# Performance work log

Measured on AMD Instinct MI355X. Metric: run time of the kernel, lower is better.

## Reference

```python
import jax, jax.numpy as jnp
import numpy as np

B, N, J, P = 64, 2048, 32, 64   # instances, ops per instance, jobs, ops per job (N = J*P)
D, H = 128, 128                 # out_size_ope, hidden_size_ope
NEG_SLOPE = 0.2


def _kaiming(key, fan_in, fan_out):
    return jax.random.normal(key, (fan_in, fan_out), jnp.float32) * np.sqrt(2.0 / fan_in)


def _mlp(x, W1, b1, W2, b2):
    # nn.Sequential(Linear, ELU, Linear)
    return jax.nn.elu(x @ W1 + b1) @ W2 + b2


def setup_inputs() -> dict:
    key = jax.random.key(0)
    ks = jax.random.split(key, 4)
    features = jax.random.normal(ks[0], (B, N, D), jnp.float32)
    job_starts = jnp.arange(J, dtype=jnp.int32) * P                      # first op of each job block
    offsets = jax.random.randint(ks[1], (B, J), 0, P)                    # current position within block
    ope_step_batch = job_starts[None, :] + offsets                       # [B, J], step_j in [start_j, end_j]
    end_ope_biases_batch = jnp.broadcast_to(job_starts + (P - 1), (B, J))
    opes_appertain_batch = jnp.broadcast_to(jnp.repeat(jnp.arange(J, dtype=jnp.int32), P)[None, :], (B, N))
    batch_idxes = jnp.arange(B, dtype=jnp.int32)
    inp = {
        'features': features,
        'discount_r': jnp.float32(0.9),
        'ope_step_batch': ope_step_batch,
        'end_ope_biases_batch': end_ope_biases_batch,
        'opes_appertain_batch': opes_appertain_batch,
        'batch_idxes': batch_idxes,
    }
    for i, nm in enumerate(['fw', 'zj', 'pr']):
        k1, k2 = jax.random.split(jax.random.fold_in(ks[2], i))
        inp[nm + '_W1'] = _kaiming(k1, D, H)
        inp[nm + '_b1'] = jnp.zeros((H,), jnp.float32)
        inp[nm + '_W2'] = _kaiming(k2, H, D)
        inp[nm + '_b2'] = jnp.zeros((D,), jnp.float32)
    return inp


def reference(features, discount_r,
              fw_W1, fw_b1, fw_W2, fw_b2,
              zj_W1, zj_b1, zj_W2, zj_b2,
              pr_W1, pr_b1, pr_W2, pr_b2,
              ope_step_batch, end_ope_biases_batch, opes_appertain_batch, batch_idxes):
    # opes_appertain_batch is accepted but unused, exactly like the torch forward.
    f32 = features.dtype
    steps = ope_step_batch[batch_idxes]        # [B, J]
    ends = end_ope_biases_batch[batch_idxes]   # [B, J]
    i = jnp.arange(N)

    # --- per-job descending update loop, vectorized ---
    # op i is updated iff step_j < i <= end_j for its job j; descending order in the
    # original means feat[i-1] is still the ORIGINAL value, so updates are independent.
    memb = (i[None, None, :] > steps[:, :, None]) & (i[None, None, :] <= ends[:, :, None])  # [B,J,N]
    updated = jnp.any(memb, axis=1)                                                         # [B,N]
    step_of = jnp.sum(jnp.where(memb, steps[:, :, None], 0), axis=1)                        # [B,N]
    rpow = discount_r ** (i[None, :] - step_of).astype(f32)                                 # r^(i - step)
    feat_prev = jnp.concatenate([jnp.zeros_like(features[:, :1]), features[:, :-1]], axis=1)
    # aggregate(MEAN): agg_f_w(feat_pre) + agg_f_w(feat_sub * r)
    cand = _mlp(features, fw_W1, fw_b1, fw_W2, fw_b2) + \
           _mlp(feat_prev * rpow[..., None], fw_W1, fw_b1, fw_W2, fw_b2)
    feat1 = jnp.where(updated[..., None], cand, features)

    # --- collect feat at each valid job's current step (step positions are never updated) ---
    collected = jax.vmap(lambda f, s: f[s])(features, steps)   # [B, J, D]
    valid = steps <= ends                                      # [B, J]
    n = jnp.sum(valid, axis=1).astype(f32)                     # [B]
    S = jnp.sum(jnp.where(valid[..., None], collected, 0.0), axis=1)  # [B, D]
    # aggregate_dif: new[j] = agg_z_j((old[j] + r * sum_{k!=j} old[k]) / n)
    mixed = (collected + discount_r * (S[:, None, :] - collected)) / n[:, None, None]
    z = _mlp(mixed, zj_W1, zj_b1, zj_W2, zj_b2)                # [B, J, D]

    # faithful replication of feat_opt[b][save_index[k]] = features_all[k]
    # (writes at op positions equal to JOB indices 0..J-1, for valid jobs)
    head = jnp.where(valid[..., None], z, feat1[:, :J, :])
    feat2 = feat1.at[:, :J, :].set(head)

    out = jax.nn.leaky_relu(_mlp(feat2, pr_W1, pr_b1, pr_W2, pr_b2), NEG_SLOPE)
    return out
```

## Files before the change

### kernel.cpp

```cpp
#include <hip/hip_runtime.h>

#define B_ 64
#define N_ 2048
#define J_ 32
#define D_ 128
#define NEG_SLOPE_ 0.2f

typedef __attribute__((ext_vector_type(4))) float f32x4;
typedef __attribute__((ext_vector_type(8))) __bf16 bf16x8;
typedef __attribute__((ext_vector_type(4))) __bf16 bf16x4;

#define ACT_NONE 0
#define ACT_ELU 1
#define ACT_LEAKY 2

template<int ACT>
__device__ __forceinline__ float apply_act(float v) {
    if constexpr (ACT == ACT_ELU)        return v > 0.f ? v : __expf(v) - 1.f;
    else if constexpr (ACT == ACT_LEAKY) return v >= 0.f ? v : NEG_SLOPE_ * v;
    else return v;
}

__device__ __forceinline__ bf16x8 frag_ld(const __bf16* src, int row, int kc) {
    return *(const bf16x8*)&src[row * D_ + ((kc ^ (row & 7)) << 3)];
}

__device__ __forceinline__ void load_wregs2(const __bf16* __restrict__ wmat,
                                            int wst, int ln, int lq, bf16x8 wr_[4][2]) {
#pragma unroll
    for (int ks = 0; ks < 4; ++ks)
#pragma unroll
        for (int mt = 0; mt < 2; ++mt)
            wr_[ks][mt] = frag_ld(wmat, wst * 32 + mt * 16 + ln, ks * 4 + lq);
}

__device__ __forceinline__ void gemmS(const __bf16* xb, const bf16x8 wr_[4][2],
                                      int ln, int lq, f32x4 acc[2][4]) {
    const f32x4 z = {0.f, 0.f, 0.f, 0.f};
#pragma unroll
    for (int mt = 0; mt < 2; ++mt)
#pragma unroll
        for (int nt = 0; nt < 4; ++nt) acc[mt][nt] = z;
#pragma unroll
    for (int ks = 0; ks < 4; ++ks) {
        const int kc = ks * 4 + lq;
        bf16x8 b[4];
#pragma unroll
        for (int nt = 0; nt < 4; ++nt) b[nt] = frag_ld(xb, nt * 16 + ln, kc);
#pragma unroll
        for (int mt = 0; mt < 2; ++mt)
#pragma unroll
            for (int nt = 0; nt < 4; ++nt)
                acc[mt][nt] = __builtin_amdgcn_mfma_f32_16x16x32_bf16(wr_[ks][mt], b[nt], acc[mt][nt], 0, 0, 0);
    }
}

__device__ __forceinline__ void gemmS32(const __bf16* xb, const bf16x8 wr_[4][2],
                                        int ln, int lq, f32x4 acc[2][2]) {
    const f32x4 z = {0.f, 0.f, 0.f, 0.f};
#pragma unroll
    for (int mt = 0; mt < 2; ++mt) { acc[mt][0] = z; acc[mt][1] = z; }
#pragma unroll
    for (int ks = 0; ks < 4; ++ks) {
        const int kc = ks * 4 + lq;
        const bf16x8 b0 = frag_ld(xb, ln, kc);
        const bf16x8 b1 = frag_ld(xb, 16 + ln, kc);
#pragma unroll
        for (int mt = 0; mt < 2; ++mt) {
            acc[mt][0] = __builtin_amdgcn_mfma_f32_16x16x32_bf16(wr_[ks][mt], b0, acc[mt][0], 0, 0, 0);
            acc[mt][1] = __builtin_amdgcn_mfma_f32_16x16x32_bf16(wr_[ks][mt], b1, acc[mt][1], 0, 0, 0);
        }
    }
}

template<int ACT>
__device__ __forceinline__ void epiS_lds(const f32x4 acc[2][4], __bf16* dst,
                                         const float* __restrict__ bias,
                                         int wst, int ln, int lq) {
#pragma unroll
    for (int mt = 0; mt < 2; ++mt) {
        const int cb = wst * 32 + mt * 16 + lq * 4;
        const f32x4 bv = *(const f32x4*)&bias[cb];
#pragma unroll
        for (int nt = 0; nt < 4; ++nt) {
            const int jr = nt * 16 + ln;
            bf16x4 o;
#pragma unroll
            for (int r = 0; r < 4; ++r)
                o[r] = (__bf16)apply_act<ACT>(acc[mt][nt][r] + bv[r]);
            *(bf16x4*)&dst[jr * D_ + (((cb >> 3) ^ (jr & 7)) << 3) + (cb & 7)] = o;
        }
    }
}

template<int ACT>
__device__ __forceinline__ void epiS32_lds(const f32x4 acc[2][2], __bf16* dst, int rowoff,
                                           const float* __restrict__ bias,
                                           int wst, int ln, int lq) {
#pragma unroll
    for (int mt = 0; mt < 2; ++mt) {
        const int cb = wst * 32 + mt * 16 + lq * 4;
        const f32x4 bv = *(const f32x4*)&bias[cb];
#pragma unroll
        for (int nt = 0; nt < 2; ++nt) {
            const int jr = rowoff + nt * 16 + ln;
            bf16x4 o;
#pragma unroll
            for (int r = 0; r < 4; ++r)
                o[r] = (__bf16)apply_act<ACT>(acc[mt][nt][r] + bv[r]);
            *(bf16x4*)&dst[jr * D_ + (((cb >> 3) ^ (jr & 7)) << 3) + (cb & 7)] = o;
        }
    }
}

__global__ __launch_bounds__(256) void k_prep(
    const float* __restrict__ w0, const float* __restrict__ w1,
    const float* __restrict__ w2, const float* __restrict__ w3,
    const float* __restrict__ w4, const float* __restrict__ w5,
    __bf16* __restrict__ wdst,
    const float* __restrict__ F, const int* __restrict__ STEP,
    const int* __restrict__ ENDB, const int* __restrict__ BIDX,
    float* __restrict__ Sbuf, int* __restrict__ nvalid) {
    const int t = threadIdx.x;
    if (blockIdx.x < 6) {
        const float* src;
        switch (blockIdx.x) {
            case 0: src = w0; break; case 1: src = w1; break; case 2: src = w2; break;
            case 3: src = w3; break; case 4: src = w4; break; default: src = w5; break;
        }
        __bf16* d = wdst + (size_t)blockIdx.x * D_ * D_;
        for (int id = t; id < D_ * 16; id += 256) {
            const int n = id >> 4, ch = id & 15;
            bf16x8 u;
#pragma unroll
            for (int j = 0; j < 8; ++j) u[j] = (__bf16)src[(ch * 8 + j) * D_ + n];
            *(bf16x8*)&d[n * D_ + ((ch ^ (n & 7)) << 3)] = u;
        }
        return;
    }
    const int b = blockIdx.x - 6;
    __shared__ int steps_s[J_];
    __shared__ int valid_s[J_];
    __shared__ int nv;
    const int bi = BIDX[b];
    if (t == 0) nv = 0;
    __syncthreads();
    if (t < J_) {
        const int s = STEP[bi * J_ + t];
        const int e = ENDB[bi * J_ + t];
        steps_s[t] = s;
        const int v = (s <= e) ? 1 : 0;
        valid_s[t] = v;
        if (v) atomicAdd(&nv, 1);
    }
    __syncthreads();
    if (t < D_) {
        float acc = 0.f;
        for (int j = 0; j < J_; ++j)
            if (valid_s[j]) acc += F[((size_t)b * N_ + steps_s[j]) * D_ + t];
        Sbuf[b * D_ + t] = acc;
    }
    if (t == 0) nvalid[b] = nv;
}

__global__ __launch_bounds__(256, 4) void k_fused(
    const float* __restrict__ F, const float* __restrict__ rp_,
    const __bf16* __restrict__ wsW,
    const float* __restrict__ fb1, const float* __restrict__ fb2,
    const float* __restrict__ zb1, const float* __restrict__ zb2,
    const float* __restrict__ pb1, const float* __restrict__ pb2,
    const int* __restrict__ STEP, const int* __restrict__ ENDB,
    const int* __restrict__ BIDX, const float* __restrict__ Sbuf,
    const int* __restrict__ nvalid, float* __restrict__ out) {
    __shared__ __bf16 xs[64 * D_];
    __shared__ __bf16 hs[64 * D_];
    __shared__ int stj[J_];
    __shared__ int ens[J_];
    __shared__ unsigned char cat[32];
    __shared__ float rsc_s[32];

    const int t = threadIdx.x;
    const int lane = t & 63, wst = t >> 6;
    const int ln = lane & 15, lq = lane >> 4;
    const int bid = blockIdx.x;
    const int b = bid >> 6, ti = bid & 63;
    const int r0 = ti * 32;
    const int bi = BIDX[b];
    if (t < J_) { stj[t] = STEP[bi * J_ + t]; ens[t] = ENDB[bi * J_ + t]; }
    __syncthreads();
    const float r = *rp_;
    if (t < 32) {
        const int i = r0 + t;
        const int j = i >> 6;
        const bool head = (i < J_) && (stj[i] <= ens[i]);
        const bool upd = (i > stj[j]) && (i <= ens[j]);
        const unsigned char c = head ? 2 : (upd ? 1 : 0);
        cat[t] = c;
        rsc_s[t] = (c == 1) ? __powf(r, (float)(i - stj[j])) : 0.f;
    }
    __syncthreads();

    const float* Fb = F + (size_t)b * N_ * D_;
    for (int id = t; id < 64 * 16; id += 256) {
        const int rr = id >> 4, ch = id & 15;
        bf16x8 u;
        if (rr < 32) {
            const float* fr = Fb + (size_t)(r0 + rr) * D_ + ch * 8;
            const float4 f0 = *(const float4*)fr, f1 = *(const float4*)(fr + 4);
            u[0] = (__bf16)f0.x; u[1] = (__bf16)f0.y; u[2] = (__bf16)f0.z; u[3] = (__bf16)f0.w;
            u[4] = (__bf16)f1.x; u[5] = (__bf16)f1.y; u[6] = (__bf16)f1.z; u[7] = (__bf16)f1.w;
        } else {
            const int lr = rr - 32;
            if (cat[lr] == 1) {
                const float s = rsc_s[lr];
                const float* fr = Fb + (size_t)(r0 + lr - 1) * D_ + ch * 8;
                const float4 f0 = *(const float4*)fr, f1 = *(const float4*)(fr + 4);
                u[0] = (__bf16)(f0.x * s); u[1] = (__bf16)(f0.y * s);
                u[2] = (__bf16)(f0.z * s); u[3] = (__bf16)(f0.w * s);
                u[4] = (__bf16)(f1.x * s); u[5] = (__bf16)(f1.y * s);
                u[6] = (__bf16)(f1.z * s); u[7] = (__bf16)(f1.w * s);
            } else {
#pragma unroll
                for (int j = 0; j < 8; ++j) u[j] = (__bf16)0.f;
            }
        }
        *(bf16x8*)&xs[rr * D_ + ((ch ^ (rr & 7)) << 3)] = u;
    }
    __syncthreads();

    {
        bf16x8 w1r[4][2];
        load_wregs2(wsW, wst, ln, lq, w1r);
        f32x4 acc[2][4];
        gemmS(xs, w1r, ln, lq, acc);
        epiS_lds<ACT_ELU>(acc, hs, fb1, wst, ln, lq);
    }
    __syncthreads();

    {
        bf16x8 w2r[4][2];
        load_wregs2(wsW + 16384, wst, ln, lq, w2r);
        f32x4 a2[2][2];
        const f32x4 z = {0.f, 0.f, 0.f, 0.f};
#pragma unroll
        for (int mt = 0; mt < 2; ++mt) { a2[mt][0] = z; a2[mt][1] = z; }
#pragma unroll
        for (int ks = 0; ks < 4; ++ks) {
            const int kc = ks * 4 + lq;
            const bf16x8 bl0 = frag_ld(hs, ln, kc);
            const bf16x8 bl1 = frag_ld(hs, 16 + ln, kc);
            const bf16x8 bh0 = frag_ld(hs, 32 + ln, kc);
            const bf16x8 bh1 = frag_ld(hs, 48 + ln, kc);
#pragma unroll
            for (int mt = 0; mt < 2; ++mt) {
                a2[mt][0] = __builtin_amdgcn_mfma_f32_16x16x32_bf16(w2r[ks][mt], bl0, a2[mt][0], 0, 0, 0);
                a2[mt][0] = __builtin_amdgcn_mfma_f32_16x16x32_bf16(w2r[ks][mt], bh0, a2[mt][0], 0, 0, 0);
                a2[mt][1] = __builtin_amdgcn_mfma_f32_16x16x32_bf16(w2r[ks][mt], bl1, a2[mt][1], 0, 0, 0);
                a2[mt][1] = __builtin_amdgcn_mfma_f32_16x16x32_bf16(w2r[ks][mt], bh1, a2[mt][1], 0, 0, 0);
            }
        }
#pragma unroll
        for (int nt = 0; nt < 2; ++nt) {
            const int row = nt * 16 + ln;
            if (cat[row] != 1) continue;
#pragma unroll
            for (int mt = 0; mt < 2; ++mt) {
                const int cb = wst * 32 + mt * 16 + lq * 4;
                const f32x4 bv = *(const f32x4*)&fb2[cb];
                bf16x4 o;
#pragma unroll
                for (int rr2 = 0; rr2 < 4; ++rr2)
                    o[rr2] = (__bf16)(a2[mt][nt][rr2] + 2.f * bv[rr2]);
                *(bf16x4*)&xs[row * D_ + (((cb >> 3) ^ (row & 7)) << 3) + (cb & 7)] = o;
            }
        }
    }

    if (ti == 0) {
        __syncthreads();
        const float n_ = (float)nvalid[b];
        const float inv = (n_ > 0.f) ? 1.f / n_ : 0.f;
        for (int id = t; id < 32 * 16; id += 256) {
            const int row = id >> 4, ch = id & 15;
            const float* cr = Fb + (size_t)stj[row] * D_ + ch * 8;
            const float4 c0 = *(const float4*)cr, c1 = *(const float4*)(cr + 4);
            const float4 s0 = *(const float4*)(Sbuf + b * D_ + ch * 8);
            const float4 s1 = *(const float4*)(Sbuf + b * D_ + ch * 8 + 4);
            bf16x8 u;
            u[0] = (__bf16)((c0.x + r * (s0.x - c0.x)) * inv);
            u[1] = (__bf16)((c0.y + r * (s0.y - c0.y)) * inv);
            u[2] = (__bf16)((c0.z + r * (s0.z - c0.z)) * inv);
            u[3] = (__bf16)((c0.w + r * (s0.w - c0.w)) * inv);
            u[4] = (__bf16)((c1.x + r * (s1.x - c1.x)) * inv);
            u[5] = (__bf16)((c1.y + r * (s1.y - c1.y)) * inv);
            u[6] = (__bf16)((c1.z + r * (s1.z - c1.z)) * inv);
            u[7] = (__bf16)((c1.w + r * (s1.w - c1.w)) * inv);
            *(bf16x8*)&hs[row * D_ + ((ch ^ (row & 7)) << 3)] = u;
        }
        __syncthreads();
        f32x4 az[2][2];
        {
            bf16x8 wza[4][2];
            load_wregs2(wsW + 4 * 16384, wst, ln, lq, wza);
            gemmS32(hs, wza, ln, lq, az);
            epiS32_lds<ACT_ELU>(az, hs, 32, zb1, wst, ln, lq);
        }
        __syncthreads();
        {
            bf16x8 wzb[4][2];
            load_wregs2(wsW + 5 * 16384, wst, ln, lq, wzb);
            gemmS32(hs + 32 * D_, wzb, ln, lq, az);
#pragma unroll
            for (int nt = 0; nt < 2; ++nt) {
                const int row = nt * 16 + ln;
                if (cat[row] != 2) continue;
#pragma unroll
                for (int mt = 0; mt < 2; ++mt) {
                    const int cb = wst * 32 + mt * 16 + lq * 4;
                    const f32x4 bv = *(const f32x4*)&zb2[cb];
                    bf16x4 o;
#pragma unroll
                    for (int rr2 = 0; rr2 < 4; ++rr2)
                        o[rr2] = (__bf16)(az[mt][nt][rr2] + bv[rr2]);
                    *(bf16x4*)&xs[row * D_ + (((cb >> 3) ^ (row & 7)) << 3) + (cb & 7)] = o;
                }
            }
        }
    }
    __syncthreads();

    {
        bf16x8 p1r[4][2];
        load_wregs2(wsW + 2 * 16384, wst, ln, lq, p1r);
        f32x4 ap[2][2];
        gemmS32(xs, p1r, ln, lq, ap);
        epiS32_lds<ACT_ELU>(ap, xs, 32, pb1, wst, ln, lq);
    }
    __syncthreads();

    {
        bf16x8 p2r[4][2];
        load_wregs2(wsW + 3 * 16384, wst, ln, lq, p2r);
        f32x4 ap[2][2];
        gemmS32(xs + 32 * D_, p2r, ln, lq, ap);
        float* outb = out + ((size_t)b * N_ + r0) * D_;
#pragma unroll
        for (int mt = 0; mt < 2; ++mt) {
            const int cb = wst * 32 + mt * 16 + lq * 4;
            const f32x4 bv = *(const f32x4*)&pb2[cb];
#pragma unroll
            for (int nt = 0; nt < 2; ++nt) {
                const int jr = nt * 16 + ln;
                f32x4 o;
#pragma unroll
                for (int rr2 = 0; rr2 < 4; ++rr2)
                    o[rr2] = apply_act<ACT_LEAKY>(ap[mt][nt][rr2] + bv[rr2]);
                *(f32x4*)&outb[(size_t)jr * D_ + cb] = o;
            }
        }
    }
}

extern "C" void kernel_launch(void* const* d_in, const int* in_sizes, int n_in,
                              void* d_out, int out_size, void* d_ws, size_t ws_size,
                              hipStream_t stream) {
    const float* F    = (const float*)d_in[0];
    const float* rp   = (const float*)d_in[1];
    const int*  STEP  = (const int*)d_in[2];
    const int*  ENDB  = (const int*)d_in[3];
    const int*  BIDX  = (const int*)d_in[5];
    const float* fwW1 = (const float*)d_in[6];
    const float* fwb1 = (const float*)d_in[7];
    const float* fwW2 = (const float*)d_in[8];
    const float* fwb2 = (const float*)d_in[9];
    const float* zjW1 = (const float*)d_in[10];
    const float* zjb1 = (const float*)d_in[11];
    const float* zjW2 = (const float*)d_in[12];
    const float* zjb2 = (const float*)d_in[13];
    const float* prW1 = (const float*)d_in[14];
    const float* prb1 = (const float*)d_in[15];
    const float* prW2 = (const float*)d_in[16];
    const float* prb2 = (const float*)d_in[17];
    float* out = (float*)d_out;

    char* ws = (char*)d_ws;
    __bf16* wsW = (__bf16*)ws;
    float* Sbuf = (float*)(ws + 393216);
    int* nvalid = (int*)(ws + 425984);

    hipLaunchKernelGGL(k_prep, dim3(70), dim3(256), 0, stream,
                       fwW1, fwW2, prW1, prW2, zjW1, zjW2, wsW,
                       F, STEP, ENDB, BIDX, Sbuf, nvalid);
    hipLaunchKernelGGL(k_fused, dim3(B_ * 64), dim3(256), 0, stream,
                       F, rp, wsW, fwb1, fwb2, zjb1, zjb2, prb1, prb2,
                       STEP, ENDB, BIDX, Sbuf, nvalid, out);
}
```

Measured before the change: 72.77 us.

## Drop second LDS buffer, reuse xs in place to raise occupancy

Removes the 16 KB hs shared buffer and runs the fw MLP as two 32-row passes that overwrite halves of xs in place, accumulating the second-layer result across passes. Extra barriers guard the in-place overwrites. The z-path likewise stages its input in the upper half of xs. Launch bounds go from 4 to 6 blocks per SM so the lower LDS footprint can give higher occupancy. The cost is more barriers, reloading the W1/W2 fragments twice, and tighter register limits.

```diff
diff --git a/kernel.cpp b/kernel.cpp
--- a/kernel.cpp
+++ b/kernel.cpp
@@ -34,32 +34,13 @@
             wr_[ks][mt] = frag_ld(wmat, wst * 32 + mt * 16 + ln, ks * 4 + lq);
 }
 
-__device__ __forceinline__ void gemmS(const __bf16* xb, const bf16x8 wr_[4][2],
-                                      int ln, int lq, f32x4 acc[2][4]) {
-    const f32x4 z = {0.f, 0.f, 0.f, 0.f};
-#pragma unroll
-    for (int mt = 0; mt < 2; ++mt)
-#pragma unroll
-        for (int nt = 0; nt < 4; ++nt) acc[mt][nt] = z;
-#pragma unroll
-    for (int ks = 0; ks < 4; ++ks) {
-        const int kc = ks * 4 + lq;
-        bf16x8 b[4];
-#pragma unroll
-        for (int nt = 0; nt < 4; ++nt) b[nt] = frag_ld(xb, nt * 16 + ln, kc);
-#pragma unroll
-        for (int mt = 0; mt < 2; ++mt)
-#pragma unroll
-            for (int nt = 0; nt < 4; ++nt)
-                acc[mt][nt] = __builtin_amdgcn_mfma_f32_16x16x32_bf16(wr_[ks][mt], b[nt], acc[mt][nt], 0, 0, 0);
-    }
-}
-
+template<bool INIT>
 __device__ __forceinline__ void gemmS32(const __bf16* xb, const bf16x8 wr_[4][2],
                                         int ln, int lq, f32x4 acc[2][2]) {
-    const f32x4 z = {0.f, 0.f, 0.f, 0.f};
-#pragma unroll
-    for (int mt = 0; mt < 2; ++mt) { acc[mt][0] = z; acc[mt][1] = z; }
+    if constexpr (INIT) {
+        const f32x4 z = {0.f, 0.f, 0.f, 0.f};
+        acc[0][0] = z; acc[0][1] = z; acc[1][0] = z; acc[1][1] = z;
+    }
 #pragma unroll
     for (int ks = 0; ks < 4; ++ks) {
         const int kc = ks * 4 + lq;
@@ -74,16 +55,16 @@
 }
 
 template<int ACT>
-__device__ __forceinline__ void epiS_lds(const f32x4 acc[2][4], __bf16* dst,
-                                         const float* __restrict__ bias,
-                                         int wst, int ln, int lq) {
+__device__ __forceinline__ void epiS32_lds(const f32x4 acc[2][2], __bf16* dst, int rowoff,
+                                           const float* __restrict__ bias,
+                                           int wst, int ln, int lq) {
 #pragma unroll
     for (int mt = 0; mt < 2; ++mt) {
         const int cb = wst * 32 + mt * 16 + lq * 4;
         const f32x4 bv = *(const f32x4*)&bias[cb];
 #pragma unroll
-        for (int nt = 0; nt < 4; ++nt) {
-            const int jr = nt * 16 + ln;
+        for (int nt = 0; nt < 2; ++nt) {
+            const int jr = rowoff + nt * 16 + ln;
             bf16x4 o;
 #pragma unroll
             for (int r = 0; r < 4; ++r)
@@ -93,22 +74,23 @@
     }
 }
 
-template<int ACT>
-__device__ __forceinline__ void epiS32_lds(const f32x4 acc[2][2], __bf16* dst, int rowoff,
-                                           const float* __restrict__ bias,
+__device__ __forceinline__ void pred_write(const f32x4 acc[2][2], __bf16* xs,
+                                           const unsigned char* cat, unsigned char want,
+                                           const float* __restrict__ bias, float bscale,
                                            int wst, int ln, int lq) {
 #pragma unroll
-    for (int mt = 0; mt < 2; ++mt) {
-        const int cb = wst * 32 + mt * 16 + lq * 4;
-        const f32x4 bv = *(const f32x4*)&bias[cb];
-#pragma unroll
-        for (int nt = 0; nt < 2; ++nt) {
-            const int jr = rowoff + nt * 16 + ln;
+    for (int nt = 0; nt < 2; ++nt) {
+        const int row = nt * 16 + ln;
+        if (cat[row] != want) continue;
+#pragma unroll
+        for (int mt = 0; mt < 2; ++mt) {
+            const int cb = wst * 32 + mt * 16 + lq * 4;
+            const f32x4 bv = *(const f32x4*)&bias[cb];
             bf16x4 o;
 #pragma unroll
             for (int r = 0; r < 4; ++r)
-                o[r] = (__bf16)apply_act<ACT>(acc[mt][nt][r] + bv[r]);
-            *(bf16x4*)&dst[jr * D_ + (((cb >> 3) ^ (jr & 7)) << 3) + (cb & 7)] = o;
+                o[r] = (__bf16)(acc[mt][nt][r] + bscale * bv[r]);
+            *(bf16x4*)&xs[row * D_ + (((cb >> 3) ^ (row & 7)) << 3) + (cb & 7)] = o;
         }
     }
 }
@@ -163,7 +145,7 @@
     if (t == 0) nvalid[b] = nv;
 }
 
-__global__ __launch_bounds__(256, 4) void k_fused(
+__global__ __launch_bounds__(256, 6) void k_fused(
     const float* __restrict__ F, const float* __restrict__ rp_,
     const __bf16* __restrict__ wsW,
     const float* __restrict__ fb1, const float* __restrict__ fb2,
@@ -173,7 +155,6 @@
     const int* __restrict__ BIDX, const float* __restrict__ Sbuf,
     const int* __restrict__ nvalid, float* __restrict__ out) {
     __shared__ __bf16 xs[64 * D_];
-    __shared__ __bf16 hs[64 * D_];
     __shared__ int stj[J_];
     __shared__ int ens[J_];
     __shared__ unsigned char cat[32];
@@ -228,52 +209,35 @@
     }
     __syncthreads();
 
+    f32x4 a2[2][2];
     {
         bf16x8 w1r[4][2];
         load_wregs2(wsW, wst, ln, lq, w1r);
-        f32x4 acc[2][4];
-        gemmS(xs, w1r, ln, lq, acc);
-        epiS_lds<ACT_ELU>(acc, hs, fb1, wst, ln, lq);
-    }
-    __syncthreads();
-
+        f32x4 acc[2][2];
+        gemmS32<true>(xs + 32 * D_, w1r, ln, lq, acc);
+        __syncthreads();
+        epiS32_lds<ACT_ELU>(acc, xs, 32, fb1, wst, ln, lq);
+    }
+    __syncthreads();
     {
         bf16x8 w2r[4][2];
         load_wregs2(wsW + 16384, wst, ln, lq, w2r);
-        f32x4 a2[2][2];
-        const f32x4 z = {0.f, 0.f, 0.f, 0.f};
-#pragma unroll
-        for (int mt = 0; mt < 2; ++mt) { a2[mt][0] = z; a2[mt][1] = z; }
-#pragma unroll
-        for (int ks = 0; ks < 4; ++ks) {
-            const int kc = ks * 4 + lq;
-            const bf16x8 bl0 = frag_ld(hs, ln, kc);
-            const bf16x8 bl1 = frag_ld(hs, 16 + ln, kc);
-            const bf16x8 bh0 = frag_ld(hs, 32 + ln, kc);
-            const bf16x8 bh1 = frag_ld(hs, 48 + ln, kc);
-#pragma unroll
-            for (int mt = 0; mt < 2; ++mt) {
-                a2[mt][0] = __builtin_amdgcn_mfma_f32_16x16x32_bf16(w2r[ks][mt], bl0, a2[mt][0], 0, 0, 0);
-                a2[mt][0] = __builtin_amdgcn_mfma_f32_16x16x32_bf16(w2r[ks][mt], bh0, a2[mt][0], 0, 0, 0);
-                a2[mt][1] = __builtin_amdgcn_mfma_f32_16x16x32_bf16(w2r[ks][mt], bl1, a2[mt][1], 0, 0, 0);
-                a2[mt][1] = __builtin_amdgcn_mfma_f32_16x16x32_bf16(w2r[ks][mt], bh1, a2[mt][1], 0, 0, 0);
-            }
-        }
-#pragma unroll
-        for (int nt = 0; nt < 2; ++nt) {
-            const int row = nt * 16 + ln;
-            if (cat[row] != 1) continue;
-#pragma unroll
-            for (int mt = 0; mt < 2; ++mt) {
-                const int cb = wst * 32 + mt * 16 + lq * 4;
-                const f32x4 bv = *(const f32x4*)&fb2[cb];
-                bf16x4 o;
-#pragma unroll
-                for (int rr2 = 0; rr2 < 4; ++rr2)
-                    o[rr2] = (__bf16)(a2[mt][nt][rr2] + 2.f * bv[rr2]);
-                *(bf16x4*)&xs[row * D_ + (((cb >> 3) ^ (row & 7)) << 3) + (cb & 7)] = o;
-            }
-        }
+        gemmS32<true>(xs + 32 * D_, w2r, ln, lq, a2);
+    }
+    __syncthreads();
+    {
+        bf16x8 w1r[4][2];
+        load_wregs2(wsW, wst, ln, lq, w1r);
+        f32x4 acc[2][2];
+        gemmS32<true>(xs, w1r, ln, lq, acc);
+        epiS32_lds<ACT_ELU>(acc, xs, 32, fb1, wst, ln, lq);
+    }
+    __syncthreads();
+    {
+        bf16x8 w2r[4][2];
+        load_wregs2(wsW + 16384, wst, ln, lq, w2r);
+        gemmS32<false>(xs + 32 * D_, w2r, ln, lq, a2);
+        pred_write(a2, xs, cat, 1, fb2, 2.f, wst, ln, lq);
     }
 
     if (ti == 0) {
@@ -295,36 +259,25 @@
             u[5] = (__bf16)((c1.y + r * (s1.y - c1.y)) * inv);
             u[6] = (__bf16)((c1.z + r * (s1.z - c1.z)) * inv);
             u[7] = (__bf16)((c1.w + r * (s1.w - c1.w)) * inv);
-            *(bf16x8*)&hs[row * D_ + ((ch ^ (row & 7)) << 3)] = u;
+            const int jr = 32 + row;
+            *(bf16x8*)&xs[jr * D_ + ((ch ^ (jr & 7)) << 3)] = u;
         }
         __syncthreads();
-        f32x4 az[2][2];
         {
             bf16x8 wza[4][2];
             load_wregs2(wsW + 4 * 16384, wst, ln, lq, wza);
-            gemmS32(hs, wza, ln, lq, az);
-            epiS32_lds<ACT_ELU>(az, hs, 32, zb1, wst, ln, lq);
+            f32x4 az[2][2];
+            gemmS32<true>(xs + 32 * D_, wza, ln, lq, az);
+            __syncthreads();
+            epiS32_lds<ACT_ELU>(az, xs, 32, zb1, wst, ln, lq);
         }
         __syncthreads();
         {
             bf16x8 wzb[4][2];
             load_wregs2(wsW + 5 * 16384, wst, ln, lq, wzb);
-            gemmS32(hs + 32 * D_, wzb, ln, lq, az);
-#pragma unroll
-            for (int nt = 0; nt < 2; ++nt) {
-                const int row = nt * 16 + ln;
-                if (cat[row] != 2) continue;
-#pragma unroll
-                for (int mt = 0; mt < 2; ++mt) {
-                    const int cb = wst * 32 + mt * 16 + lq * 4;
-                    const f32x4 bv = *(const f32x4*)&zb2[cb];
-                    bf16x4 o;
-#pragma unroll
-                    for (int rr2 = 0; rr2 < 4; ++rr2)
-                        o[rr2] = (__bf16)(az[mt][nt][rr2] + bv[rr2]);
-                    *(bf16x4*)&xs[row * D_ + (((cb >> 3) ^ (row & 7)) << 3) + (cb & 7)] = o;
-                }
-            }
+            f32x4 az[2][2];
+            gemmS32<true>(xs + 32 * D_, wzb, ln, lq, az);
+            pred_write(az, xs, cat, 2, zb2, 1.f, wst, ln, lq);
         }
     }
     __syncthreads();
@@ -333,16 +286,15 @@
         bf16x8 p1r[4][2];
         load_wregs2(wsW + 2 * 16384, wst, ln, lq, p1r);
         f32x4 ap[2][2];
-        gemmS32(xs, p1r, ln, lq, ap);
+        gemmS32<true>(xs, p1r, ln, lq, ap);
         epiS32_lds<ACT_ELU>(ap, xs, 32, pb1, wst, ln, lq);
     }
     __syncthreads();
-
     {
         bf16x8 p2r[4][2];
         load_wregs2(wsW + 3 * 16384, wst, ln, lq, p2r);
         f32x4 ap[2][2];
-        gemmS32(xs + 32 * D_, p2r, ln, lq, ap);
+        gemmS32<true>(xs + 32 * D_, p2r, ln, lq, ap);
         float* outb = out + ((size_t)b * N_ + r0) * D_;
 #pragma unroll
         for (int mt = 0; mt < 2; ++mt) {
```

Result: slower. 99.15 us (+36.3%).
